# Optimization experiments

Measured on AMD Instinct MI355X. Metric: run time of the kernel, lower is better.

The kernel has to match this reference:

```python
import jax, jax.numpy as jnp
import numpy as np

CH = 512      # input channels
V = 320       # codewords per group
G = 2         # groups
CV_DIM = 256  # codevector_dim (wav2vec2 default)
D = CV_DIM // G
TAU = 2.0     # gumbel temperature


def setup_inputs() -> dict:
    key = jax.random.key(0)
    k1, k2, k3, k4 = jax.random.split(key, 4)
    B, T = 32, 1024
    x = jax.random.normal(k1, (B, T, CH), jnp.float32)
    W_proj = jax.random.normal(k2, (CH, G * V), jnp.float32) / np.sqrt(CH)
    b_proj = jnp.zeros((G * V,), jnp.float32)
    codevectors = jax.random.normal(k3, (G, V, D), jnp.float32) * 0.02
    # uniform noise, transformed to Gumbel inside reference
    u_noise = jax.random.uniform(k4, (B, T, G, V), jnp.float32,
                                 minval=1e-6, maxval=1.0 - 1e-6)
    return {"x": x, "W_proj": W_proj, "b_proj": b_proj,
            "codevectors": codevectors, "u_noise": u_noise}


def reference(x, W_proj, b_proj, codevectors, u_noise):
    B, T, _ = x.shape
    # projection to per-group logits: [B,T,G,V]
    logits = (x @ W_proj + b_proj).reshape(B, T, G, V)
    # gumbel-softmax (hard, straight-through)
    g = -jnp.log(-jnp.log(u_noise))
    soft = jax.nn.softmax((logits + g) / TAU, axis=-1)
    hard = jax.nn.one_hot(jnp.argmax(soft, axis=-1), V, dtype=soft.dtype)
    st = hard + soft - jax.lax.stop_gradient(soft)
    # combine selected codewords per group, concat groups -> [B,T,CV_DIM]
    out = jnp.einsum('btgv,gvd->btgd', st, codevectors).reshape(B, T, G * D)
    return out
```

## Files before the change

### kernel.cpp

```cpp
#include <hip/hip_runtime.h>
#include <cmath>

namespace {

typedef _Float16 half8 __attribute__((ext_vector_type(8)));
typedef _Float16 half4v __attribute__((ext_vector_type(4)));
typedef float f32x4 __attribute__((ext_vector_type(4)));

constexpr int M_TOTAL = 32 * 1024;
constexpr int K_CH    = 512;
constexpr int NV      = 640;
constexpr int D_CV    = 128;
constexpr int NSLOT   = 10;

constexpr int BM = 128, BN = 64, BK = 32;
constexpr int NTILE  = NV / BN;
constexpr int NPANEL = M_TOTAL / BM;
constexpr int NBLK   = NTILE * NPANEL;
constexpr int KT     = K_CH / BK;

constexpr int LBUF = 12288;

constexpr float LO_SCALE = 4096.0f;
constexpr float LO_INV   = 1.0f / 4096.0f;

__device__ __forceinline__ void gld16(const void* g, void* l) {
  __builtin_amdgcn_global_load_lds(
      (__attribute__((address_space(1))) void*)g,
      (__attribute__((address_space(3))) void*)l, 16, 0, 0);
}

__global__ __launch_bounds__(256)
void prep_w(const float* __restrict__ W, _Float16* __restrict__ Wth,
            _Float16* __restrict__ Wtl)
{
  __shared__ float tile[32][33];
  const int bk = blockIdx.x & 15;
  const int bn = blockIdx.x >> 4;
  const int k0 = bk * 32, n0 = bn * 32;
  const int t = threadIdx.x;
  const int nn = t & 31, kk = t >> 5;
  #pragma unroll
  for (int p = 0; p < 4; ++p)
    tile[kk + p * 8][nn] = W[(size_t)(k0 + kk + p * 8) * NV + n0 + nn];
  __syncthreads();
  const int kx = t & 31, nx = t >> 5;
  #pragma unroll
  for (int p = 0; p < 4; ++p) {
    const float v = tile[kx][nx + p * 8];
    const _Float16 h = (_Float16)v;
    const _Float16 l = (_Float16)((v - (float)h) * LO_SCALE);
    const size_t o = (size_t)(n0 + nx + p * 8) * K_CH + k0 + kx;
    Wth[o] = h;
    Wtl[o] = l;
  }
}

__global__ __launch_bounds__(256)
void prep_x(const float* __restrict__ x, _Float16* __restrict__ Xh,
            _Float16* __restrict__ Xl)
{
  const size_t i = ((size_t)blockIdx.x * 256 + threadIdx.x) * 2;
  #pragma unroll
  for (int j = 0; j < 2; ++j) {
    const float4 v = reinterpret_cast<const float4*>(x)[i + j];
    const float* pv = &v.x;
    half4v h, l;
    #pragma unroll
    for (int e = 0; e < 4; ++e) {
      const _Float16 hh = (_Float16)pv[e];
      h[e] = hh;
      l[e] = (_Float16)((pv[e] - (float)hh) * LO_SCALE);
    }
    reinterpret_cast<half4v*>(Xh)[i + j] = h;
    reinterpret_cast<half4v*>(Xl)[i + j] = l;
  }
}

__global__ __launch_bounds__(256, 3)
void gvq_mfma6(const _Float16* __restrict__ Xh, const _Float16* __restrict__ Xl,
               const _Float16* __restrict__ Wth, const _Float16* __restrict__ Wtl,
               const float* __restrict__ bias, const float* __restrict__ u,
               float* __restrict__ pval, int* __restrict__ pidx)
{
  __shared__ __align__(16) _Float16 lds[2 * LBUF];

  const int chunk = NBLK / 8;
  const int nid   = (blockIdx.x % 8) * chunk + blockIdx.x / 8;
  const int panel = nid / NTILE, ntile = nid % NTILE;
  const int m0 = panel * BM, n0 = ntile * BN;

  const int t    = threadIdx.x;
  const int wv   = t >> 6, lane = t & 63;
  const int li   = lane & 15, q = lane >> 4;

  const int r0 = t >> 2;
  const int gc = (t & 3) ^ ((t >> 3) & 3);
  const _Float16* pxh = Xh  + (size_t)(m0 + r0) * K_CH + gc * 8;
  const _Float16* pxl = Xl  + (size_t)(m0 + r0) * K_CH + gc * 8;
  const _Float16* pbh = Wth + (size_t)(n0 + r0) * K_CH + gc * 8;
  const _Float16* pbl = Wtl + (size_t)(n0 + r0) * K_CH + gc * 8;

  f32x4 acc1[2][4];
  f32x4 acc2[2][4];
  #pragma unroll
  for (int i = 0; i < 2; ++i)
    #pragma unroll
    for (int j = 0; j < 4; ++j) {
      acc1[i][j] = (f32x4){0.f, 0.f, 0.f, 0.f};
      acc2[i][j] = (f32x4){0.f, 0.f, 0.f, 0.f};
    }

  auto stage = [&](int kt, int b) {
    const int ko = kt * BK;
    _Float16* L = &lds[b * LBUF];
    gld16(pxh + ko,                      L + 0     + wv * 512);
    gld16(pxh + (size_t)64 * K_CH + ko,  L + 2048  + wv * 512);
    gld16(pxl + ko,                      L + 4096  + wv * 512);
    gld16(pxl + (size_t)64 * K_CH + ko,  L + 6144  + wv * 512);
    gld16(pbh + ko,                      L + 8192  + wv * 512);
    gld16(pbl + ko,                      L + 10240 + wv * 512);
  };

  const int soff = ((q ^ ((li >> 1) & 3)) << 3);
  const int arow = (wv * 32 + li) * 32;
  const int brow = li * 32;

  stage(0, 0);
  asm volatile("s_waitcnt vmcnt(0)" ::: "memory");
  __builtin_amdgcn_s_barrier();
  __builtin_amdgcn_sched_barrier(0);

  #pragma unroll
  for (int kt = 0; kt < KT; ++kt) {
    const int cur = kt & 1;
    if (kt + 1 < KT) stage(kt + 1, cur ^ 1);

    const _Float16* L = &lds[cur * LBUF];
    half8 bh[4], bl[4], ah[2], al[2];
    #pragma unroll
    for (int fn = 0; fn < 4; ++fn) {
      bh[fn] = *reinterpret_cast<const half8*>(L + 8192  + brow + fn * 512 + soff);
      bl[fn] = *reinterpret_cast<const half8*>(L + 10240 + brow + fn * 512 + soff);
    }
    #pragma unroll
    for (int fm = 0; fm < 2; ++fm) {
      ah[fm] = *reinterpret_cast<const half8*>(L + arow + fm * 512 + soff);
      al[fm] = *reinterpret_cast<const half8*>(L + 4096 + arow + fm * 512 + soff);
    }
    __builtin_amdgcn_s_setprio(1);
    #pragma unroll
    for (int fm = 0; fm < 2; ++fm)
      #pragma unroll
      for (int fn = 0; fn < 4; ++fn) {
        acc1[fm][fn] = __builtin_amdgcn_mfma_f32_16x16x32_f16(
            ah[fm], bh[fn], acc1[fm][fn], 0, 0, 0);
        acc2[fm][fn] = __builtin_amdgcn_mfma_f32_16x16x32_f16(
            ah[fm], bl[fn], acc2[fm][fn], 0, 0, 0);
        acc2[fm][fn] = __builtin_amdgcn_mfma_f32_16x16x32_f16(
            al[fm], bh[fn], acc2[fm][fn], 0, 0, 0);
      }
    __builtin_amdgcn_s_setprio(0);

    if (kt + 1 < KT) {
      asm volatile("s_waitcnt vmcnt(0)" ::: "memory");
      __builtin_amdgcn_s_barrier();
      __builtin_amdgcn_sched_barrier(0);
    }
  }

  const int colbase = n0 + li;
  float bb[4];
  #pragma unroll
  for (int fn = 0; fn < 4; ++fn) bb[fn] = bias[colbase + fn * 16];

  const int slot = ntile;
  #pragma unroll
  for (int fm = 0; fm < 2; ++fm) {
    #pragma unroll
    for (int r = 0; r < 4; ++r) {
      const int m = m0 + wv * 32 + fm * 16 + q * 4 + r;
      float bv = -INFINITY;
      int   bi = 0x7fffffff;
      #pragma unroll
      for (int fn = 0; fn < 4; ++fn) {
        const float uu  = u[(size_t)m * NV + colbase + fn * 16];
        const float g   = -__logf(-__logf(uu));
        const float val = acc1[fm][fn][r] + acc2[fm][fn][r] * LO_INV
                          + bb[fn] + g;
        const int   n   = colbase + fn * 16;
        if (val > bv) { bv = val; bi = n; }
      }
      #pragma unroll
      for (int s = 1; s <= 8; s <<= 1) {
        const float ov = __shfl_xor(bv, s);
        const int   oi = __shfl_xor(bi, s);
        if (ov > bv || (ov == bv && oi < bi)) { bv = ov; bi = oi; }
      }
      if (li == 0) {
        pval[(size_t)m * NSLOT + slot] = bv;
        pidx[(size_t)m * NSLOT + slot] = bi;
      }
    }
  }
}

__global__ __launch_bounds__(256)
void gvq_gather(const float* __restrict__ pval,
                const int*   __restrict__ pidx,
                const float* __restrict__ cv,
                float* __restrict__ out)
{
  const int tid  = threadIdx.x;
  const int w    = tid >> 6;
  const int lane = tid & 63;
  const int m    = blockIdx.x * 4 + w;
  const int g    = lane >> 5;

  const float* pv = &pval[(size_t)m * NSLOT + g * 5];
  const int*   pi = &pidx[(size_t)m * NSLOT + g * 5];
  float bv = pv[0];
  int   bi = pi[0];
  #pragma unroll
  for (int s = 1; s < 5; ++s) {
    const float v = pv[s];
    const int   i = pi[s];
    if (v > bv || (v == bv && i < bi)) { bv = v; bi = i; }
  }
  const float4 src = *reinterpret_cast<const float4*>(
      &cv[(size_t)bi * D_CV + (lane & 31) * 4]);
  *reinterpret_cast<float4*>(&out[(size_t)m * 256 + lane * 4]) = src;
}

}

extern "C" void kernel_launch(void* const* d_in, const int* in_sizes, int n_in,
                              void* d_out, int out_size, void* d_ws, size_t ws_size,
                              hipStream_t stream)
{
  const float* x    = (const float*)d_in[0];
  const float* W    = (const float*)d_in[1];
  const float* bias = (const float*)d_in[2];
  const float* cv   = (const float*)d_in[3];
  const float* u    = (const float*)d_in[4];
  float* out = (float*)d_out;

  _Float16* Wth  = (_Float16*)d_ws;
  _Float16* Wtl  = Wth + (size_t)NV * K_CH;
  float*    pval = (float*)(Wtl + (size_t)NV * K_CH);
  int*      pidx = (int*)(pval + (size_t)M_TOTAL * NSLOT);
  _Float16* Xh   = (_Float16*)(pidx + (size_t)M_TOTAL * NSLOT);
  _Float16* Xl   = Xh + (size_t)M_TOTAL * K_CH;

  hipLaunchKernelGGL(prep_w, dim3(320), dim3(256), 0, stream, W, Wth, Wtl);
  hipLaunchKernelGGL(prep_x, dim3(8192), dim3(256), 0, stream, x, Xh, Xl);
  hipLaunchKernelGGL(gvq_mfma6, dim3(NBLK), dim3(256), 0, stream,
                     Xh, Xl, Wth, Wtl, bias, u, pval, pidx);
  hipLaunchKernelGGL(gvq_gather, dim3(M_TOTAL / 4), dim3(256), 0, stream,
                     pval, pidx, cv, out);
}
```

Baseline: 137.2 us.

## Load A fragments directly to registers and prefetch B two stages ahead

The GEMM kernel stops staging the X (A) tiles through LDS and has each wave load its own A fragments from global memory straight into registers, with even and odd register sets. Only the W (B) tiles still go through LDS, and their prefetch runs two k-steps ahead, with partial vmcnt waits and a second barrier so a buffer is refilled only after it has been read. This cuts LDS footprint and LDS traffic and deepens the prefetch pipeline. The cost is more VGPR pressure and uncoalesced per-lane global reads of A, with no cross-wave reuse. A is not shared across waves anyway.

```diff
diff --git a/kernel.cpp b/kernel.cpp
--- a/kernel.cpp
+++ b/kernel.cpp
@@ -18,8 +18,6 @@
 constexpr int NPANEL = M_TOTAL / BM;
 constexpr int NBLK   = NTILE * NPANEL;
 constexpr int KT     = K_CH / BK;
-
-constexpr int LBUF = 12288;
 
 constexpr float LO_SCALE = 4096.0f;
 constexpr float LO_INV   = 1.0f / 4096.0f;
@@ -78,12 +76,12 @@
 }
 
 __global__ __launch_bounds__(256, 3)
-void gvq_mfma6(const _Float16* __restrict__ Xh, const _Float16* __restrict__ Xl,
+void gvq_mfma7(const _Float16* __restrict__ Xh, const _Float16* __restrict__ Xl,
                const _Float16* __restrict__ Wth, const _Float16* __restrict__ Wtl,
                const float* __restrict__ bias, const float* __restrict__ u,
                float* __restrict__ pval, int* __restrict__ pidx)
 {
-  __shared__ __align__(16) _Float16 lds[2 * LBUF];
+  __shared__ __align__(16) _Float16 lds[2][4096];
 
   const int chunk = NBLK / 8;
   const int nid   = (blockIdx.x % 8) * chunk + blockIdx.x / 8;
@@ -96,10 +94,13 @@
 
   const int r0 = t >> 2;
   const int gc = (t & 3) ^ ((t >> 3) & 3);
-  const _Float16* pxh = Xh  + (size_t)(m0 + r0) * K_CH + gc * 8;
-  const _Float16* pxl = Xl  + (size_t)(m0 + r0) * K_CH + gc * 8;
   const _Float16* pbh = Wth + (size_t)(n0 + r0) * K_CH + gc * 8;
   const _Float16* pbl = Wtl + (size_t)(n0 + r0) * K_CH + gc * 8;
+
+  const _Float16* pah0 = Xh + (size_t)(m0 + wv * 32 + li) * K_CH + q * 8;
+  const _Float16* pah1 = Xh + (size_t)(m0 + wv * 32 + 16 + li) * K_CH + q * 8;
+  const _Float16* pal0 = Xl + (size_t)(m0 + wv * 32 + li) * K_CH + q * 8;
+  const _Float16* pal1 = Xl + (size_t)(m0 + wv * 32 + 16 + li) * K_CH + q * 8;
 
   f32x4 acc1[2][4];
   f32x4 acc2[2][4];
@@ -111,44 +112,20 @@
       acc2[i][j] = (f32x4){0.f, 0.f, 0.f, 0.f};
     }
 
-  auto stage = [&](int kt, int b) {
+  auto stageB = [&](int kt, int b) {
     const int ko = kt * BK;
-    _Float16* L = &lds[b * LBUF];
-    gld16(pxh + ko,                      L + 0     + wv * 512);
-    gld16(pxh + (size_t)64 * K_CH + ko,  L + 2048  + wv * 512);
-    gld16(pxl + ko,                      L + 4096  + wv * 512);
-    gld16(pxl + (size_t)64 * K_CH + ko,  L + 6144  + wv * 512);
-    gld16(pbh + ko,                      L + 8192  + wv * 512);
-    gld16(pbl + ko,                      L + 10240 + wv * 512);
+    gld16(pbh + ko, &lds[b][wv * 512]);
+    gld16(pbl + ko, &lds[b][2048 + wv * 512]);
   };
-
-  const int soff = ((q ^ ((li >> 1) & 3)) << 3);
-  const int arow = (wv * 32 + li) * 32;
-  const int brow = li * 32;
-
-  stage(0, 0);
-  asm volatile("s_waitcnt vmcnt(0)" ::: "memory");
-  __builtin_amdgcn_s_barrier();
-  __builtin_amdgcn_sched_barrier(0);
-
-  #pragma unroll
-  for (int kt = 0; kt < KT; ++kt) {
-    const int cur = kt & 1;
-    if (kt + 1 < KT) stage(kt + 1, cur ^ 1);
-
-    const _Float16* L = &lds[cur * LBUF];
-    half8 bh[4], bl[4], ah[2], al[2];
-    #pragma unroll
-    for (int fn = 0; fn < 4; ++fn) {
-      bh[fn] = *reinterpret_cast<const half8*>(L + 8192  + brow + fn * 512 + soff);
-      bl[fn] = *reinterpret_cast<const half8*>(L + 10240 + brow + fn * 512 + soff);
-    }
-    #pragma unroll
-    for (int fm = 0; fm < 2; ++fm) {
-      ah[fm] = *reinterpret_cast<const half8*>(L + arow + fm * 512 + soff);
-      al[fm] = *reinterpret_cast<const half8*>(L + 4096 + arow + fm * 512 + soff);
-    }
-    __builtin_amdgcn_s_setprio(1);
+  half8 ahE[2], alE[2], ahO[2], alO[2];
+  auto loadA = [&](int kt, half8* ah, half8* al) {
+    const int ko = kt * BK;
+    ah[0] = *reinterpret_cast<const half8*>(pah0 + ko);
+    ah[1] = *reinterpret_cast<const half8*>(pah1 + ko);
+    al[0] = *reinterpret_cast<const half8*>(pal0 + ko);
+    al[1] = *reinterpret_cast<const half8*>(pal1 + ko);
+  };
+  auto mfma_blk = [&](half8* ah, half8* al, half8* bh, half8* bl) {
     #pragma unroll
     for (int fm = 0; fm < 2; ++fm)
       #pragma unroll
@@ -160,12 +137,41 @@
         acc2[fm][fn] = __builtin_amdgcn_mfma_f32_16x16x32_f16(
             al[fm], bh[fn], acc2[fm][fn], 0, 0, 0);
       }
+  };
+
+  const int soff = ((q ^ ((li >> 1) & 3)) << 3);
+
+  stageB(0, 0); loadA(0, ahE, alE);
+  stageB(1, 1); loadA(1, ahO, alO);
+
+  #pragma unroll
+  for (int kt = 0; kt < KT; ++kt) {
+    const int cur = kt & 1;
+    if (kt < KT - 1) asm volatile("s_waitcnt vmcnt(10)" ::: "memory");
+    else             asm volatile("s_waitcnt vmcnt(0)"  ::: "memory");
+    __builtin_amdgcn_s_barrier();
+
+    const _Float16* L = &lds[cur][0];
+    half8 bh[4], bl[4];
+    #pragma unroll
+    for (int fn = 0; fn < 4; ++fn) {
+      bh[fn] = *reinterpret_cast<const half8*>(L + fn * 512 + li * 32 + soff);
+      bl[fn] = *reinterpret_cast<const half8*>(L + 2048 + fn * 512 + li * 32 + soff);
+    }
+    asm volatile("s_waitcnt lgkmcnt(0)" ::: "memory");
+    __builtin_amdgcn_sched_barrier(0);
+    __builtin_amdgcn_s_barrier();
+
+    if (kt + 2 < KT) stageB(kt + 2, cur);
+
+    __builtin_amdgcn_s_setprio(1);
+    if (cur == 0) mfma_blk(ahE, alE, bh, bl);
+    else          mfma_blk(ahO, alO, bh, bl);
     __builtin_amdgcn_s_setprio(0);
 
-    if (kt + 1 < KT) {
-      asm volatile("s_waitcnt vmcnt(0)" ::: "memory");
-      __builtin_amdgcn_s_barrier();
-      __builtin_amdgcn_sched_barrier(0);
+    if (kt + 2 < KT) {
+      if (cur == 0) loadA(kt + 2, ahE, alE);
+      else          loadA(kt + 2, ahO, alO);
     }
   }
 
@@ -254,7 +260,7 @@
 
   hipLaunchKernelGGL(prep_w, dim3(320), dim3(256), 0, stream, W, Wth, Wtl);
   hipLaunchKernelGGL(prep_x, dim3(8192), dim3(256), 0, stream, x, Xh, Xl);
-  hipLaunchKernelGGL(gvq_mfma6, dim3(NBLK), dim3(256), 0, stream,
+  hipLaunchKernelGGL(gvq_mfma7, dim3(NBLK), dim3(256), 0, stream,
                      Xh, Xl, Wth, Wtl, bias, u, pval, pidx);
   hipLaunchKernelGGL(gvq_gather, dim3(M_TOTAL / 4), dim3(256), 0, stream,
                      pval, pidx, cv, out);
```

After: 144.5 us. +5.3%, slower.
